# Kernel tuning notes

Measured on AMD Instinct MI355X. Metric: run time of the kernel, lower is better.

The kernel has to match this reference:

```python
import jax, jax.numpy as jnp
import numpy as np

N = 10000      # nodes
E = 160000     # edges
D_IN = 512
D_H = 512
P_DROP = 0.2


def _glorot(key, shape):
    lim = float(np.sqrt(6.0 / (shape[0] + shape[1])))
    return jax.random.uniform(key, shape, jnp.float32, -lim, lim)


def setup_inputs() -> dict:
    key = jax.random.key(0)
    ks = jax.random.split(key, 8)
    h = jax.random.normal(ks[0], (N, D_IN), jnp.float32)
    src = jax.random.randint(ks[1], (E,), 0, N)
    dst = jax.random.randint(ks[2], (E,), 0, N)
    edge_weight = jax.random.uniform(ks[3], (E,), jnp.float32)
    W0 = _glorot(ks[4], (D_IN, D_H))
    W1 = _glorot(ks[5], (D_H, D_H))
    W2 = _glorot(ks[6], (D_H, D_H))
    b0 = jnp.zeros((D_H,), jnp.float32)
    b1 = jnp.zeros((D_H,), jnp.float32)
    b2 = jnp.zeros((D_H,), jnp.float32)
    return dict(h=h, src=src, dst=dst, edge_weight=edge_weight,
                W0=W0, b0=b0, W1=W1, b1=b1, W2=W2, b2=b2)


def _dropout(x, key):
    keep = jax.random.bernoulli(key, 1.0 - P_DROP, x.shape)
    return jnp.where(keep, x / (1.0 - P_DROP), 0.0)


def _graph_conv(x, src, dst, ew, W, b, act):
    # DGL GraphConv, norm='both', weight=True, bias=True, with edge_weight.
    ones = jnp.ones((src.shape[0],), x.dtype)
    deg_out = jnp.maximum(jax.ops.segment_sum(ones, src, num_segments=N), 1.0)
    deg_in = jnp.maximum(jax.ops.segment_sum(ones, dst, num_segments=N), 1.0)
    x = x * (deg_out ** -0.5)[:, None]          # src norm
    msg = x[src] * ew[:, None]                  # [E, D] gather + edge weight
    agg = jax.ops.segment_sum(msg, dst, num_segments=N)  # scatter-add
    out = (agg @ W) * (deg_in ** -0.5)[:, None] + b
    return act(out) if act is not None else out


def reference(h, src, dst, edge_weight, W0, b0, W1, b1, W2, b2):
    dk = jax.random.split(jax.random.key(42), 3)
    x = _dropout(h, dk[0])
    x = _graph_conv(x, src, dst, edge_weight, W0, b0, jax.nn.elu)
    x = _dropout(x, dk[1])
    x = _graph_conv(x, src, dst, edge_weight, W1, b1, jax.nn.elu)
    x = _dropout(x, dk[2])
    x = _graph_conv(x, src, dst, edge_weight, W2, b2, None)
    return x
```

## Files before the change

kernel.cpp:

```cpp
#include <hip/hip_runtime.h>
#include <stdint.h>

#define N_NODES 10000
#define N_EDGES 160000
#define D 512
#define TOT (N_NODES * D)
#define M_PAD 10112
#define MASK_DW (TOT / 32)

typedef _Float16 h8 __attribute__((ext_vector_type(8)));
typedef float f4 __attribute__((ext_vector_type(4)));

__host__ __device__ inline uint32_t rotl32(uint32_t v, int r) {
    return (v << r) | (v >> (32 - r));
}

__host__ __device__ inline void tf2x32(uint32_t k0, uint32_t k1,
                                       uint32_t& x0, uint32_t& x1) {
    uint32_t k2 = k0 ^ k1 ^ 0x1BD11BDAu;
    x0 += k0; x1 += k1;
    x0 += x1; x1 = rotl32(x1, 13); x1 ^= x0;
    x0 += x1; x1 = rotl32(x1, 15); x1 ^= x0;
    x0 += x1; x1 = rotl32(x1, 26); x1 ^= x0;
    x0 += x1; x1 = rotl32(x1,  6); x1 ^= x0;
    x0 += k1; x1 += k2 + 1u;
    x0 += x1; x1 = rotl32(x1, 17); x1 ^= x0;
    x0 += x1; x1 = rotl32(x1, 29); x1 ^= x0;
    x0 += x1; x1 = rotl32(x1, 16); x1 ^= x0;
    x0 += x1; x1 = rotl32(x1, 24); x1 ^= x0;
    x0 += k2; x1 += k0 + 2u;
    x0 += x1; x1 = rotl32(x1, 13); x1 ^= x0;
    x0 += x1; x1 = rotl32(x1, 15); x1 ^= x0;
    x0 += x1; x1 = rotl32(x1, 26); x1 ^= x0;
    x0 += x1; x1 = rotl32(x1,  6); x1 ^= x0;
    x0 += k0; x1 += k1 + 3u;
    x0 += x1; x1 = rotl32(x1, 17); x1 ^= x0;
    x0 += x1; x1 = rotl32(x1, 29); x1 ^= x0;
    x0 += x1; x1 = rotl32(x1, 16); x1 ^= x0;
    x0 += x1; x1 = rotl32(x1, 24); x1 ^= x0;
    x0 += k1; x1 += k2 + 4u;
    x0 += x1; x1 = rotl32(x1, 13); x1 ^= x0;
    x0 += x1; x1 = rotl32(x1, 15); x1 ^= x0;
    x0 += x1; x1 = rotl32(x1, 26); x1 ^= x0;
    x0 += x1; x1 = rotl32(x1,  6); x1 ^= x0;
    x0 += k2; x1 += k0 + 5u;
}

__device__ __forceinline__ float dropout_gate(uint32_t k0, uint32_t k1, uint32_t j) {
    uint32_t c0 = 0u, c1 = j;
    tf2x32(k0, k1, c0, c1);
    uint32_t bits = c0 ^ c1;
    float u = __uint_as_float((bits >> 9) | 0x3f800000u) - 1.0f;
    return (u < 0.8f) ? 1.0f : 0.0f;
}

__global__ __launch_bounds__(256)
void mask_kernel(uint32_t* __restrict__ mask, uint32_t k0a, uint32_t k1a,
                 uint32_t k0b, uint32_t k1b) {
    int t = blockIdx.x * 256 + threadIdx.x;
    int layer = (t >= MASK_DW) ? 1 : 0;
    uint32_t k0 = layer ? k0b : k0a;
    uint32_t k1 = layer ? k1b : k1a;
    uint32_t base = (uint32_t)(layer ? t - MASK_DW : t) * 32u;
    uint32_t m = 0;
#pragma unroll
    for (int i = 0; i < 32; ++i) {
        uint32_t c0 = 0u, c1 = base + (uint32_t)i;
        tf2x32(k0, k1, c0, c1);
        uint32_t bits = c0 ^ c1;
        float u = __uint_as_float((bits >> 9) | 0x3f800000u) - 1.0f;
        m |= (u < 0.8f ? 1u : 0u) << i;
    }
    mask[t] = m;
}

__global__ void hist_kernel(const int* __restrict__ src, const int* __restrict__ dst,
                            int* __restrict__ deg_out, int* __restrict__ deg_in) {
    int e = blockIdx.x * 256 + threadIdx.x;
    if (e >= N_EDGES) return;
    atomicAdd(&deg_out[src[e]], 1);
    atomicAdd(&deg_in[dst[e]], 1);
}

__global__ __launch_bounds__(1024)
void scan_kernel(const int* __restrict__ deg_in, const int* __restrict__ deg_out,
                 int* __restrict__ row_ptr,
                 float* __restrict__ rn_in, float* __restrict__ rn_out) {
    __shared__ int wsum[16];
    __shared__ int base_s;
    int tid = threadIdx.x;
    int lane = tid & 63, wv = tid >> 6;
    if (tid == 0) base_s = 0;
    __syncthreads();
    for (int start = 0; start < N_NODES; start += 1024) {
        int i = start + tid;
        int v = (i < N_NODES) ? deg_in[i] : 0;
        int s = v;
#pragma unroll
        for (int off = 1; off < 64; off <<= 1) {
            int t = __shfl_up(s, off, 64);
            if (lane >= off) s += t;
        }
        if (lane == 63) wsum[wv] = s;
        __syncthreads();
        if (wv == 0 && lane < 16) {
            int ws = wsum[lane];
#pragma unroll
            for (int off = 1; off < 16; off <<= 1) {
                int t = __shfl_up(ws, off, 64);
                if (lane >= off) ws += t;
            }
            wsum[lane] = ws;
        }
        __syncthreads();
        if (i < N_NODES) {
            int prefix = base_s + ((wv > 0) ? wsum[wv - 1] : 0) + (s - v);
            row_ptr[i] = prefix;
            rn_in[i]  = 1.0f / sqrtf(fmaxf((float)v, 1.0f));
            rn_out[i] = 1.0f / sqrtf(fmaxf((float)deg_out[i], 1.0f));
        }
        __syncthreads();
        if (tid == 0) base_s += wsum[15];
        __syncthreads();
    }
    if (tid == 0) row_ptr[N_NODES] = base_s;
}

__global__ void fill_kernel(const int* __restrict__ src, const int* __restrict__ dst,
                            const float* __restrict__ ew, const int* __restrict__ row_ptr,
                            int* __restrict__ cursor, int2* __restrict__ csr) {
    int e = blockIdx.x * 256 + threadIdx.x;
    if (e >= N_EDGES) return;
    int v = dst[e];
    int pos = atomicAdd(&cursor[v], 1);
    int idx = row_ptr[v] + pos;
    csr[idx] = make_int2(src[e], __float_as_int(ew[e]));
}

__global__ __launch_bounds__(256)
void wconvert_kernel(const float* __restrict__ W0, const float* __restrict__ W1,
                     const float* __restrict__ W2, _Float16* __restrict__ Wt) {
    __shared__ float tile[64][65];
    const float* W = (blockIdx.z == 0) ? W0 : (blockIdx.z == 1) ? W1 : W2;
    _Float16* T = Wt + (size_t)blockIdx.z * 512 * 512;
    int r0 = blockIdx.y * 64, c0 = blockIdx.x * 64;
    int t = threadIdx.x;
    int c = t & 63, rq = t >> 6;
#pragma unroll
    for (int i = 0; i < 16; ++i) {
        int r = rq + i * 4;
        tile[r][c] = W[(size_t)(r0 + r) * 512 + c0 + c];
    }
    __syncthreads();
    int k = t & 63, nq = t >> 6;
#pragma unroll
    for (int i = 0; i < 16; ++i) {
        int n = nq + i * 4;
        T[(size_t)(c0 + n) * 512 + r0 + k] = (_Float16)tile[k][n];
    }
}

__global__ __launch_bounds__(256)
void dropout_kernel(const float* __restrict__ x, _Float16* __restrict__ y,
                    const float* __restrict__ rn_out, uint32_t k0, uint32_t k1) {
    int t = blockIdx.x * 256 + threadIdx.x;
    int j = t * 4;
    if (j >= TOT) return;
    float4 xv = *(const float4*)&x[j];
    float w = rn_out[j >> 9];
    _Float16 r[4];
    uint32_t jj = (uint32_t)j;
#pragma unroll
    for (int i = 0; i < 4; ++i) {
        float g = dropout_gate(k0, k1, jj + (uint32_t)i);
        float xi = (&xv.x)[i];
        r[i] = (_Float16)(g * (xi / 0.8f) * w);
    }
    *(ushort4*)&y[j] = *(ushort4*)r;
}

__global__ __launch_bounds__(256)
void aggregate_kernel(const _Float16* __restrict__ y, const int* __restrict__ row_ptr,
                      const int2* __restrict__ csr, _Float16* __restrict__ agg) {
    int node = blockIdx.x * 4 + (threadIdx.x >> 6);
    int lane = threadIdx.x & 63;
    if (node >= N_NODES) return;
    int beg = row_ptr[node], end = row_ptr[node + 1];
    float acc[8] = {0, 0, 0, 0, 0, 0, 0, 0};
    int k = beg;
    for (; k + 7 < end; k += 8) {
        h8 a[8];
        float w[8];
#pragma unroll
        for (int q = 0; q < 8; ++q) {
            int2 e = csr[k + q];
            a[q] = *(const h8*)&y[(size_t)e.x * 512 + lane * 8];
            w[q] = __int_as_float(e.y);
        }
#pragma unroll
        for (int q = 0; q < 8; ++q)
#pragma unroll
            for (int i = 0; i < 8; ++i) acc[i] += w[q] * (float)a[q][i];
    }
    for (; k + 3 < end; k += 4) {
        h8 a[4];
        float w[4];
#pragma unroll
        for (int q = 0; q < 4; ++q) {
            int2 e = csr[k + q];
            a[q] = *(const h8*)&y[(size_t)e.x * 512 + lane * 8];
            w[q] = __int_as_float(e.y);
        }
#pragma unroll
        for (int q = 0; q < 4; ++q)
#pragma unroll
            for (int i = 0; i < 8; ++i) acc[i] += w[q] * (float)a[q][i];
    }
    for (; k < end; ++k) {
        int2 e0 = csr[k];
        float w0 = __int_as_float(e0.y);
        h8 a = *(const h8*)&y[(size_t)e0.x * 512 + lane * 8];
#pragma unroll
        for (int i = 0; i < 8; ++i) acc[i] += w0 * (float)a[i];
    }
    _Float16 r[8];
#pragma unroll
    for (int i = 0; i < 8; ++i) r[i] = (_Float16)acc[i];
    *(h8*)&agg[(size_t)node * 512 + lane * 8] = *(h8*)r;
}

#define GBK 32
#define LDA 40
__global__ __launch_bounds__(256)
void gemm_kernel(const _Float16* __restrict__ A, const _Float16* __restrict__ Wt,
                 const float* __restrict__ bias, const float* __restrict__ rn_in,
                 const float* __restrict__ rn_out, const uint32_t* __restrict__ mask,
                 _Float16* __restrict__ yout, float* __restrict__ fout, int mode) {
    __shared__ _Float16 As[128 * LDA];
    int tid = threadIdx.x;
    int wv = tid >> 6, lane = tid & 63;

    int f = blockIdx.x + blockIdx.y * 8;
    int T = (f & 7) * 79 + (f >> 3);
    int row0 = (T >> 3) * 128, col0 = (T & 7) * 64;

    int wr = wv >> 1, wc = wv & 1;

    f4 acc[4][2];
#pragma unroll
    for (int i = 0; i < 4; ++i)
#pragma unroll
        for (int j = 0; j < 2; ++j) acc[i][j] = (f4){0.f, 0.f, 0.f, 0.f};

    int srow = tid >> 2;
    int sseg = (tid & 3) * 8;
    const _Float16* gA0 = A + (size_t)(row0 + srow) * 512 + sseg;
    const _Float16* gA1 = gA0 + (size_t)64 * 512;
    _Float16* wA0 = &As[srow * LDA + sseg];
    _Float16* wA1 = &As[(64 + srow) * LDA + sseg];

    int kf = (lane >> 4) * 8;
    const _Float16* fa = &As[(wr * 64 + (lane & 15)) * LDA + kf];
    const _Float16* gB0 = Wt + (size_t)(col0 + wc * 32 + (lane & 15)) * 512 + kf;
    const _Float16* gB1 = gB0 + (size_t)16 * 512;

    h8 ra0 = *(const h8*)gA0;
    h8 ra1 = *(const h8*)gA1;
    h8 rb0 = *(const h8*)gB0;
    h8 rb1 = *(const h8*)gB1;

    for (int kk = 0; kk < 512; kk += GBK) {
        *(h8*)wA0 = ra0;
        *(h8*)wA1 = ra1;
        h8 bf0 = rb0, bf1 = rb1;
        __syncthreads();
        if (kk + GBK < 512) {
            ra0 = *(const h8*)(gA0 + kk + GBK);
            ra1 = *(const h8*)(gA1 + kk + GBK);
            rb0 = *(const h8*)(gB0 + kk + GBK);
            rb1 = *(const h8*)(gB1 + kk + GBK);
        }
        h8 af[4];
#pragma unroll
        for (int mt = 0; mt < 4; ++mt) af[mt] = *(const h8*)(fa + mt * 16 * LDA);
#pragma unroll
        for (int mt = 0; mt < 4; ++mt) {
            acc[mt][0] = __builtin_amdgcn_mfma_f32_16x16x32_f16(af[mt], bf0,
                                                                acc[mt][0], 0, 0, 0);
            acc[mt][1] = __builtin_amdgcn_mfma_f32_16x16x32_f16(af[mt], bf1,
                                                                acc[mt][1], 0, 0, 0);
        }
        __syncthreads();
    }

    int mbase = row0 + wr * 64;
    int nbase = col0 + wc * 32;
#pragma unroll
    for (int mt = 0; mt < 4; ++mt) {
#pragma unroll
        for (int nt = 0; nt < 2; ++nt) {
            int gr0 = mbase + mt * 16 + (lane >> 4) * 4;
            int gc = nbase + nt * 16 + (lane & 15);
            float bcol = bias[gc];
#pragma unroll
            for (int i = 0; i < 4; ++i) {
                int gr = gr0 + i;
                if (gr >= N_NODES) continue;
                float v = acc[mt][nt][i] * rn_in[gr] + bcol;
                if (mode == 0) {
                    v = (v > 0.f) ? v : expm1f(v);
                    uint32_t m = mask[gr * 16 + (gc >> 5)];
                    float keep = (float)((m >> (gc & 31)) & 1u);
                    v = keep * (v / 0.8f) * rn_out[gr];
                    yout[(size_t)gr * 512 + gc] = (_Float16)v;
                } else {
                    fout[(size_t)gr * 512 + gc] = v;
                }
            }
        }
    }
}

extern "C" void kernel_launch(void* const* d_in, const int* in_sizes, int n_in,
                              void* d_out, int out_size, void* d_ws, size_t ws_size,
                              hipStream_t stream) {
    const float* h   = (const float*)d_in[0];
    const int*   src = (const int*)d_in[1];
    const int*   dst = (const int*)d_in[2];
    const float* ew  = (const float*)d_in[3];
    const float* W0  = (const float*)d_in[4];
    const float* b0  = (const float*)d_in[5];
    const float* W1  = (const float*)d_in[6];
    const float* b1  = (const float*)d_in[7];
    const float* W2  = (const float*)d_in[8];
    const float* b2  = (const float*)d_in[9];
    const float* bl[3] = {b0, b1, b2};
    float* out = (float*)d_out;

    char* ws = (char*)d_ws;
    _Float16* y16  = (_Float16*)ws; ws += (size_t)TOT * 2;
    _Float16* aggF = (_Float16*)ws; ws += (size_t)M_PAD * 512 * 2;
    _Float16* Wt   = (_Float16*)ws; ws += (size_t)3 * 512 * 512 * 2;
    uint32_t* mask = (uint32_t*)ws; ws += (size_t)2 * MASK_DW * 4;
    int* degi_in  = (int*)ws;  ws += N_NODES * 4;
    int* degi_out = (int*)ws;  ws += N_NODES * 4;
    int* cursor   = (int*)ws;  ws += N_NODES * 4;
    int* row_ptr  = (int*)ws;  ws += (N_NODES + 1) * 4;
    ws = (char*)(((uintptr_t)ws + 15) & ~(uintptr_t)15);
    int2* csr     = (int2*)ws; ws += (size_t)N_EDGES * 8;
    float* rn_in  = (float*)ws; ws += N_NODES * 4;
    float* rn_out = (float*)ws; ws += N_NODES * 4;

    hipMemsetAsync(degi_in, 0, 3 * N_NODES * 4, stream);

    uint32_t dk[3][2];
    for (int i = 0; i < 3; ++i) {
        uint32_t c0 = 0u, c1 = (uint32_t)i;
        tf2x32(0u, 42u, c0, c1);
        dk[i][0] = c0; dk[i][1] = c1;
    }

    mask_kernel<<<(2 * MASK_DW) / 256, 256, 0, stream>>>(mask, dk[1][0], dk[1][1],
                                                         dk[2][0], dk[2][1]);
    hist_kernel<<<(N_EDGES + 255) / 256, 256, 0, stream>>>(src, dst, degi_out, degi_in);
    scan_kernel<<<1, 1024, 0, stream>>>(degi_in, degi_out, row_ptr, rn_in, rn_out);
    fill_kernel<<<(N_EDGES + 255) / 256, 256, 0, stream>>>(src, dst, ew, row_ptr,
                                                           cursor, csr);
    wconvert_kernel<<<dim3(8, 8, 3), 256, 0, stream>>>(W0, W1, W2, Wt);

    dropout_kernel<<<(TOT / 4 + 255) / 256, 256, 0, stream>>>(h, y16, rn_out,
                                                              dk[0][0], dk[0][1]);
    for (int l = 0; l < 3; ++l) {
        aggregate_kernel<<<N_NODES / 4, 256, 0, stream>>>(y16, row_ptr, csr, aggF);
        int mode = (l < 2) ? 0 : 1;
        gemm_kernel<<<dim3(8, M_PAD / 128), 256, 0, stream>>>(
            aggF, Wt + (size_t)l * 512 * 512, bl[l], rn_in, rn_out,
            mask + (size_t)l * MASK_DW, y16, out, mode);
    }
}
```

Baseline: 324.6 us.

## Fuse neighbor aggregation and GEMM into one per-layer kernel with ping-pong buffers

Merges the aggregate and GEMM kernels into a single layer kernel. Each 1024-thread block gathers 64 node rows into LDS, then multiplies them by the full 512-wide weight matrix using MFMA. This removes the fp16 round-trip of the aggregated matrix through global memory and one launch per layer, and ping-pong y buffers avoid read/write hazards. In exchange, each block re-reads all of W from global/L2 with no LDS staging, and there are only 157 blocks, which may underfill the GPU.

Result: no change. 324.8 us (+0.1%).

```diff
diff --git a/kernel.cpp b/kernel.cpp
--- a/kernel.cpp
+++ b/kernel.cpp
@@ -5,8 +5,9 @@
 #define N_EDGES 160000
 #define D 512
 #define TOT (N_NODES * D)
-#define M_PAD 10112
 #define MASK_DW (TOT / 32)
+#define FM 64
+#define LDAF 520
 
 typedef _Float16 h8 __attribute__((ext_vector_type(8)));
 typedef float f4 __attribute__((ext_vector_type(4)));
@@ -179,72 +180,67 @@
     *(ushort4*)&y[j] = *(ushort4*)r;
 }
 
-__global__ __launch_bounds__(256)
-void aggregate_kernel(const _Float16* __restrict__ y, const int* __restrict__ row_ptr,
-                      const int2* __restrict__ csr, _Float16* __restrict__ agg) {
-    int node = blockIdx.x * 4 + (threadIdx.x >> 6);
-    int lane = threadIdx.x & 63;
-    if (node >= N_NODES) return;
-    int beg = row_ptr[node], end = row_ptr[node + 1];
-    float acc[8] = {0, 0, 0, 0, 0, 0, 0, 0};
-    int k = beg;
-    for (; k + 7 < end; k += 8) {
-        h8 a[8];
-        float w[8];
-#pragma unroll
-        for (int q = 0; q < 8; ++q) {
-            int2 e = csr[k + q];
-            a[q] = *(const h8*)&y[(size_t)e.x * 512 + lane * 8];
-            w[q] = __int_as_float(e.y);
-        }
-#pragma unroll
-        for (int q = 0; q < 8; ++q)
-#pragma unroll
-            for (int i = 0; i < 8; ++i) acc[i] += w[q] * (float)a[q][i];
-    }
-    for (; k + 3 < end; k += 4) {
-        h8 a[4];
-        float w[4];
-#pragma unroll
-        for (int q = 0; q < 4; ++q) {
-            int2 e = csr[k + q];
-            a[q] = *(const h8*)&y[(size_t)e.x * 512 + lane * 8];
-            w[q] = __int_as_float(e.y);
-        }
-#pragma unroll
-        for (int q = 0; q < 4; ++q)
-#pragma unroll
-            for (int i = 0; i < 8; ++i) acc[i] += w[q] * (float)a[q][i];
-    }
-    for (; k < end; ++k) {
-        int2 e0 = csr[k];
-        float w0 = __int_as_float(e0.y);
-        h8 a = *(const h8*)&y[(size_t)e0.x * 512 + lane * 8];
-#pragma unroll
-        for (int i = 0; i < 8; ++i) acc[i] += w0 * (float)a[i];
-    }
-    _Float16 r[8];
-#pragma unroll
-    for (int i = 0; i < 8; ++i) r[i] = (_Float16)acc[i];
-    *(h8*)&agg[(size_t)node * 512 + lane * 8] = *(h8*)r;
-}
-
-#define GBK 32
-#define LDA 40
-__global__ __launch_bounds__(256)
-void gemm_kernel(const _Float16* __restrict__ A, const _Float16* __restrict__ Wt,
-                 const float* __restrict__ bias, const float* __restrict__ rn_in,
-                 const float* __restrict__ rn_out, const uint32_t* __restrict__ mask,
-                 _Float16* __restrict__ yout, float* __restrict__ fout, int mode) {
-    __shared__ _Float16 As[128 * LDA];
+__global__ __launch_bounds__(1024, 4)
+void layer_kernel(const _Float16* __restrict__ yin, const int* __restrict__ row_ptr,
+                  const int2* __restrict__ csr, const _Float16* __restrict__ Wt,
+                  const float* __restrict__ bias, const float* __restrict__ rn_in,
+                  const float* __restrict__ rn_out, const uint32_t* __restrict__ mask,
+                  _Float16* __restrict__ yout, float* __restrict__ fout, int mode) {
+    __shared__ _Float16 As[FM * LDAF];
     int tid = threadIdx.x;
     int wv = tid >> 6, lane = tid & 63;
-
-    int f = blockIdx.x + blockIdx.y * 8;
-    int T = (f & 7) * 79 + (f >> 3);
-    int row0 = (T >> 3) * 128, col0 = (T & 7) * 64;
-
-    int wr = wv >> 1, wc = wv & 1;
+    int row0 = blockIdx.x * FM;
+
+#pragma unroll 1
+    for (int nn = 0; nn < 4; ++nn) {
+        int ln = wv * 4 + nn;
+        int node = row0 + ln;
+        float acc[8] = {0, 0, 0, 0, 0, 0, 0, 0};
+        if (node < N_NODES) {
+            int beg = row_ptr[node], end = row_ptr[node + 1];
+            int k = beg;
+            for (; k + 7 < end; k += 8) {
+                h8 a[8];
+                float w[8];
+#pragma unroll
+                for (int q = 0; q < 8; ++q) {
+                    int2 e = csr[k + q];
+                    a[q] = *(const h8*)&yin[(size_t)e.x * 512 + lane * 8];
+                    w[q] = __int_as_float(e.y);
+                }
+#pragma unroll
+                for (int q = 0; q < 8; ++q)
+#pragma unroll
+                    for (int i = 0; i < 8; ++i) acc[i] += w[q] * (float)a[q][i];
+            }
+            for (; k + 3 < end; k += 4) {
+                h8 a[4];
+                float w[4];
+#pragma unroll
+                for (int q = 0; q < 4; ++q) {
+                    int2 e = csr[k + q];
+                    a[q] = *(const h8*)&yin[(size_t)e.x * 512 + lane * 8];
+                    w[q] = __int_as_float(e.y);
+                }
+#pragma unroll
+                for (int q = 0; q < 4; ++q)
+#pragma unroll
+                    for (int i = 0; i < 8; ++i) acc[i] += w[q] * (float)a[q][i];
+            }
+            for (; k < end; ++k) {
+                int2 e0 = csr[k];
+                float w0 = __int_as_float(e0.y);
+                h8 a = *(const h8*)&yin[(size_t)e0.x * 512 + lane * 8];
+#pragma unroll
+                for (int i = 0; i < 8; ++i) acc[i] += w0 * (float)a[i];
+            }
+        }
+        _Float16 r[8];
+#pragma unroll
+        for (int i = 0; i < 8; ++i) r[i] = (_Float16)acc[i];
+        *(h8*)&As[ln * LDAF + lane * 8] = *(h8*)r;
+    }
+    __syncthreads();
 
     f4 acc[4][2];
 #pragma unroll
@@ -252,37 +248,20 @@
 #pragma unroll
         for (int j = 0; j < 2; ++j) acc[i][j] = (f4){0.f, 0.f, 0.f, 0.f};
 
-    int srow = tid >> 2;
-    int sseg = (tid & 3) * 8;
-    const _Float16* gA0 = A + (size_t)(row0 + srow) * 512 + sseg;
-    const _Float16* gA1 = gA0 + (size_t)64 * 512;
-    _Float16* wA0 = &As[srow * LDA + sseg];
-    _Float16* wA1 = &As[(64 + srow) * LDA + sseg];
-
     int kf = (lane >> 4) * 8;
-    const _Float16* fa = &As[(wr * 64 + (lane & 15)) * LDA + kf];
-    const _Float16* gB0 = Wt + (size_t)(col0 + wc * 32 + (lane & 15)) * 512 + kf;
+    const _Float16* fa = &As[(lane & 15) * LDAF + kf];
+    int col0 = wv * 32;
+    const _Float16* gB0 = Wt + (size_t)(col0 + (lane & 15)) * 512 + kf;
     const _Float16* gB1 = gB0 + (size_t)16 * 512;
 
-    h8 ra0 = *(const h8*)gA0;
-    h8 ra1 = *(const h8*)gA1;
-    h8 rb0 = *(const h8*)gB0;
-    h8 rb1 = *(const h8*)gB1;
-
-    for (int kk = 0; kk < 512; kk += GBK) {
-        *(h8*)wA0 = ra0;
-        *(h8*)wA1 = ra1;
-        h8 bf0 = rb0, bf1 = rb1;
-        __syncthreads();
-        if (kk + GBK < 512) {
-            ra0 = *(const h8*)(gA0 + kk + GBK);
-            ra1 = *(const h8*)(gA1 + kk + GBK);
-            rb0 = *(const h8*)(gB0 + kk + GBK);
-            rb1 = *(const h8*)(gB1 + kk + GBK);
-        }
-        h8 af[4];
-#pragma unroll
-        for (int mt = 0; mt < 4; ++mt) af[mt] = *(const h8*)(fa + mt * 16 * LDA);
+#pragma unroll 4
+    for (int kk = 0; kk < 512; kk += 32) {
+        h8 af[4], bf0, bf1;
+        bf0 = *(const h8*)(gB0 + kk);
+        bf1 = *(const h8*)(gB1 + kk);
+#pragma unroll
+        for (int mt = 0; mt < 4; ++mt)
+            af[mt] = *(const h8*)(fa + mt * 16 * LDAF + kk);
 #pragma unroll
         for (int mt = 0; mt < 4; ++mt) {
             acc[mt][0] = __builtin_amdgcn_mfma_f32_16x16x32_f16(af[mt], bf0,
@@ -290,17 +269,14 @@
             acc[mt][1] = __builtin_amdgcn_mfma_f32_16x16x32_f16(af[mt], bf1,
                                                                 acc[mt][1], 0, 0, 0);
         }
-        __syncthreads();
-    }
-
-    int mbase = row0 + wr * 64;
-    int nbase = col0 + wc * 32;
+    }
+
 #pragma unroll
     for (int mt = 0; mt < 4; ++mt) {
 #pragma unroll
         for (int nt = 0; nt < 2; ++nt) {
-            int gr0 = mbase + mt * 16 + (lane >> 4) * 4;
-            int gc = nbase + nt * 16 + (lane & 15);
+            int gr0 = row0 + mt * 16 + (lane >> 4) * 4;
+            int gc = col0 + nt * 16 + (lane & 15);
             float bcol = bias[gc];
 #pragma unroll
             for (int i = 0; i < 4; ++i) {
@@ -338,8 +314,8 @@
     float* out = (float*)d_out;
 
     char* ws = (char*)d_ws;
-    _Float16* y16  = (_Float16*)ws; ws += (size_t)TOT * 2;
-    _Float16* aggF = (_Float16*)ws; ws += (size_t)M_PAD * 512 * 2;
+    _Float16* yA   = (_Float16*)ws; ws += (size_t)TOT * 2;
+    _Float16* yB   = (_Float16*)ws; ws += (size_t)TOT * 2;
     _Float16* Wt   = (_Float16*)ws; ws += (size_t)3 * 512 * 512 * 2;
     uint32_t* mask = (uint32_t*)ws; ws += (size_t)2 * MASK_DW * 4;
     int* degi_in  = (int*)ws;  ws += N_NODES * 4;
@@ -368,13 +344,15 @@
                                                            cursor, csr);
     wconvert_kernel<<<dim3(8, 8, 3), 256, 0, stream>>>(W0, W1, W2, Wt);
 
-    dropout_kernel<<<(TOT / 4 + 255) / 256, 256, 0, stream>>>(h, y16, rn_out,
+    dropout_kernel<<<(TOT / 4 + 255) / 256, 256, 0, stream>>>(h, yA, rn_out,
                                                               dk[0][0], dk[0][1]);
-    for (int l = 0; l < 3; ++l) {
-        aggregate_kernel<<<N_NODES / 4, 256, 0, stream>>>(y16, row_ptr, csr, aggF);
-        int mode = (l < 2) ? 0 : 1;
-        gemm_kernel<<<dim3(8, M_PAD / 128), 256, 0, stream>>>(
-            aggF, Wt + (size_t)l * 512 * 512, bl[l], rn_in, rn_out,
-            mask + (size_t)l * MASK_DW, y16, out, mode);
-    }
-}
+    const int NBLK = (N_NODES + FM - 1) / FM;
+    layer_kernel<<<NBLK, 1024, 0, stream>>>(yA, row_ptr, csr, Wt, bl[0],
+                                            rn_in, rn_out, mask, yB, out, 0);
+    layer_kernel<<<NBLK, 1024, 0, stream>>>(yB, row_ptr, csr, Wt + (size_t)512 * 512,
+                                            bl[1], rn_in, rn_out, mask + MASK_DW,
+                                            yA, out, 0);
+    layer_kernel<<<NBLK, 1024, 0, stream>>>(yA, row_ptr, csr, Wt + (size_t)2 * 512 * 512,
+                                            bl[2], rn_in, rn_out, nullptr,
+                                            nullptr, out, 1);
+}
```
